# Kernel optimization log

Measured on AMD Instinct MI355X. Metric: run time of the kernel, lower is better.

Reference implementation:

```python
import jax, jax.numpy as jnp
import numpy as np

N_NODES = 100000
LN_EPS = 1e-5


def gcn_conv(x, src, dst, W, b, num_nodes):
    """PyG-style GCNConv: x@W, add self-loops, symmetric D^-1/2 A D^-1/2 aggregation, + bias."""
    h = x @ W  # [N, out]
    loop = jnp.arange(num_nodes, dtype=src.dtype)
    s = jnp.concatenate([src, loop])
    d = jnp.concatenate([dst, loop])
    deg = jax.ops.segment_sum(jnp.ones_like(d, dtype=h.dtype), d, num_segments=num_nodes)
    dinv = jnp.where(deg > 0, jax.lax.rsqrt(deg), 0.0)
    norm = dinv[s] * dinv[d]  # [E+N]
    msg = h[s] * norm[:, None]
    return jax.ops.segment_sum(msg, d, num_segments=num_nodes) + b


def layer_norm(x, g, b):
    mu = jnp.mean(x, axis=-1, keepdims=True)
    var = jnp.mean(jnp.square(x - mu), axis=-1, keepdims=True)
    return (x - mu) * jax.lax.rsqrt(var + LN_EPS) * g + b


def setup_inputs() -> dict:
    key = jax.random.key(0)
    ks = jax.random.split(key, 12)
    N, D, OUT = N_NODES, 128, 16
    E, EL = 1600000, 500000
    x = jnp.arange(N, dtype=jnp.int64) if jax.config.jax_enable_x64 else jnp.arange(N, dtype=jnp.int32)
    edge_index = jax.random.randint(ks[0], (2, E), 0, N)
    edge_label_index = jax.random.randint(ks[1], (2, EL), 0, N)
    s = 1.0 / np.sqrt(D)
    return {
        "x": x,
        "edge_index": edge_index,
        "edge_label_index": edge_label_index,
        "emb_table": jax.random.normal(ks[2], (N, D), jnp.float32),
        "W1": jax.random.normal(ks[3], (D, D), jnp.float32) * s,
        "b1": jnp.zeros((D,), jnp.float32),
        "ln_g": jnp.ones((D,), jnp.float32),
        "ln_b": jnp.zeros((D,), jnp.float32),
        "W2": jax.random.normal(ks[4], (D, OUT), jnp.float32) * s,
        "b2": jnp.zeros((OUT,), jnp.float32),
        "L1": jax.random.normal(ks[5], (2 * OUT, 16), jnp.float32) * (1.0 / np.sqrt(2 * OUT)),
        "bl1": jnp.zeros((16,), jnp.float32),
        "L2": jax.random.normal(ks[6], (16, 1), jnp.float32) * 0.25,
        "bl2": jnp.zeros((1,), jnp.float32),
    }


def reference(x, edge_index, edge_label_index, emb_table, W1, b1, ln_g, ln_b, W2, b2, L1, bl1, L2, bl2):
    src, dst = edge_index[0], edge_index[1]
    h = emb_table[x]  # embed + squeeze -> [N, D]
    # conv 1: GCN -> relu -> (dropout, eval: identity) -> LayerNorm
    h = gcn_conv(h, src, dst, W1, b1, N_NODES)
    h = layer_norm(jax.nn.relu(h), ln_g, ln_b)
    # conv 2: emb is the pre-activation output (what encode returns)
    z = gcn_conv(h, src, dst, W2, b2, N_NODES)  # [N, 16]
    # decode: gather-concat + small MLP (dropout eval: identity)
    feat = jnp.concatenate([z[edge_label_index[0]], z[edge_label_index[1]]], axis=-1)  # [EL, 32]
    out = jax.nn.relu(feat @ L1 + bl1) if False else (feat @ L1 + bl1)  # Sequential has no activation
    out = out @ L2 + bl2  # [EL, 1]
    return out
```

## Files before the change

### kernel.cpp

```cpp
#include <hip/hip_runtime.h>


typedef __attribute__((ext_vector_type(8))) __bf16 bf16x8;
typedef __attribute__((ext_vector_type(4))) __bf16 bf16x4;
typedef __attribute__((ext_vector_type(4))) float f32x4;

static __device__ __forceinline__ unsigned f2bf1(float x) {
  unsigned u = __float_as_uint(x);
  return (u + 0x7FFFu + ((u >> 16) & 1u)) >> 16;
}
static __device__ __forceinline__ unsigned packbf2(float lo, float hi) {
  return f2bf1(lo) | (f2bf1(hi) << 16);
}
static __device__ __forceinline__ float bfl(unsigned u) { return __uint_as_float(u << 16); }
static __device__ __forceinline__ float bfh(unsigned u) { return __uint_as_float(u & 0xFFFF0000u); }

__global__ __launch_bounds__(256) void prep_wfrag(const float* __restrict__ W1,
                                                  ushort* __restrict__ wfrag) {
  int idx = blockIdx.x * 256 + threadIdx.x;
  int j = idx & 7, lane = (idx >> 3) & 63, ct = (idx >> 9) & 7, kt = idx >> 12;
  int k = kt * 32 + (lane >> 4) * 8 + j;
  int col = ct * 16 + (lane & 15);
  __bf16 h = (__bf16)W1[k * 128 + col];
  wfrag[idx] = __builtin_bit_cast(ushort, h);
}

__global__ __launch_bounds__(256) void bucket_edges(const int* __restrict__ src,
                                                    const int* __restrict__ dst,
                                                    int E, int NB,
                                                    int* __restrict__ qcur,
                                                    uint2* __restrict__ queues,
                                                    int qcap) {
  __shared__ int lcnt[128];
  __shared__ int lbase[128];
  int t = threadIdx.x;
  int CH = (E + gridDim.x - 1) / gridDim.x;
  int beg = blockIdx.x * CH;
  int end = min(E, beg + CH);
  for (int i = t; i < NB; i += 256) lcnt[i] = 0;
  __syncthreads();
  for (int e = beg + t; e < end; e += 256) atomicAdd(&lcnt[dst[e] >> 10], 1);
  __syncthreads();
  for (int i = t; i < NB; i += 256) {
    lbase[i] = atomicAdd(&qcur[i], lcnt[i]);
    lcnt[i] = 0;
  }
  __syncthreads();
  for (int e = beg + t; e < end; e += 256) {
    int d = dst[e];
    int p = d >> 10;
    int pos = lbase[p] + atomicAdd(&lcnt[p], 1);
    if (pos < qcap) queues[(size_t)p * qcap + pos] = make_uint2((unsigned)src[e], (unsigned)d);
  }
}

__global__ __launch_bounds__(1024) void scatter_ell(const uint2* __restrict__ queues,
                                                    const int* __restrict__ qcur,
                                                    int qcap, int* __restrict__ cnt,
                                                    float* __restrict__ dinv,
                                                    int* __restrict__ colsrc, int N) {
  __shared__ int lcnt[1024];
  int b = blockIdx.x, t = threadIdx.x;
  lcnt[t] = 0;
  __syncthreads();
  int len = min(qcur[b], qcap);
  const uint2* q = queues + (size_t)b * qcap;
  int lo = b << 10;
  for (int i = t; i < len; i += 1024) {
    uint2 e = q[i];
    int pos = atomicAdd(&lcnt[e.y - lo], 1);
    if (pos < 64) colsrc[(size_t)e.y * 64 + pos] = (int)e.x;
  }
  __syncthreads();
  int node = lo + t;
  if (node < N) {
    int c = min(lcnt[t], 64);
    cnt[node] = c;
    dinv[node] = rsqrtf((float)(c + 1));
  }
}

__global__ __launch_bounds__(256) void gemm1_mfma(
    const int* __restrict__ x, const float* __restrict__ emb,
    const ushort* __restrict__ wfrag, const float* __restrict__ dinv,
    unsigned* __restrict__ h1b, int N) {
  __shared__ alignas(16) ushort Wlds[16384];
  int t = threadIdx.x;
  for (int i = t; i < 2048; i += 256)
    ((uint4*)Wlds)[i] = ((const uint4*)wfrag)[i];
  __syncthreads();
  int w = t >> 6, lane = t & 63;
  int row0 = blockIdx.x * 128 + w * 32;
  int rB = lane & 15, kg = lane >> 4;
  int n0 = row0 + rB, n1 = row0 + 16 + rB;
  const float* e0 = emb + (size_t)x[min(n0, N - 1)] * 128 + kg * 8;
  const float* e1 = emb + (size_t)x[min(n1, N - 1)] * 128 + kg * 8;
  f32x4 acc[2][8];
#pragma unroll
  for (int g = 0; g < 2; ++g)
#pragma unroll
    for (int ct = 0; ct < 8; ++ct) acc[g][ct] = (f32x4)(0.f);
#pragma unroll
  for (int kt = 0; kt < 4; ++kt) {
    float4 p0 = *(const float4*)(e0 + kt * 32);
    float4 p1 = *(const float4*)(e0 + kt * 32 + 4);
    float4 q0 = *(const float4*)(e1 + kt * 32);
    float4 q1 = *(const float4*)(e1 + kt * 32 + 4);
    bf16x8 fb0, fb1;
    fb0[0] = (__bf16)p0.x; fb0[1] = (__bf16)p0.y; fb0[2] = (__bf16)p0.z; fb0[3] = (__bf16)p0.w;
    fb0[4] = (__bf16)p1.x; fb0[5] = (__bf16)p1.y; fb0[6] = (__bf16)p1.z; fb0[7] = (__bf16)p1.w;
    fb1[0] = (__bf16)q0.x; fb1[1] = (__bf16)q0.y; fb1[2] = (__bf16)q0.z; fb1[3] = (__bf16)q0.w;
    fb1[4] = (__bf16)q1.x; fb1[5] = (__bf16)q1.y; fb1[6] = (__bf16)q1.z; fb1[7] = (__bf16)q1.w;
#pragma unroll
    for (int ct = 0; ct < 8; ++ct) {
      bf16x8 wv = *(const bf16x8*)&Wlds[((kt * 8 + ct) * 64 + lane) * 8];
      acc[0][ct] = __builtin_amdgcn_mfma_f32_16x16x32_bf16(wv, fb0, acc[0][ct], 0, 0, 0);
      acc[1][ct] = __builtin_amdgcn_mfma_f32_16x16x32_bf16(wv, fb1, acc[1][ct], 0, 0, 0);
    }
  }
#pragma unroll
  for (int g = 0; g < 2; ++g) {
    int node = row0 + g * 16 + rB;
    if (node < N) {
      float dv = dinv[node];
#pragma unroll
      for (int ct = 0; ct < 8; ++ct) {
        f32x4 a = acc[g][ct];
        bf16x4 o;
        o[0] = (__bf16)(a[0] * dv); o[1] = (__bf16)(a[1] * dv);
        o[2] = (__bf16)(a[2] * dv); o[3] = (__bf16)(a[3] * dv);
        *(uint2*)&h1b[(size_t)node * 64 + ct * 8 + kg * 2] = __builtin_bit_cast(uint2, o);
      }
    }
  }
}

__global__ __launch_bounds__(256) void agg1_ln(const unsigned* __restrict__ h1b,
                                               const int* __restrict__ cnt_a,
                                               const int* __restrict__ colsrc,
                                               const float* __restrict__ dinv,
                                               const float* __restrict__ b1,
                                               const float* __restrict__ lng,
                                               const float* __restrict__ lnb,
                                               unsigned* __restrict__ h2b, int N) {
  int v = blockIdx.x * 4 + (threadIdx.x >> 6);
  int lane = threadIdx.x & 63;
  if (v >= N) return;
  int g = lane >> 4, dq = lane & 15;
  const uint4* tb = (const uint4*)h1b;
  int myidx = colsrc[(size_t)v * 64 + lane];
  int cnt = cnt_a[v];
  float a0 = 0.f, a1 = 0.f, a2 = 0.f, a3 = 0.f;
  float a4 = 0.f, a5 = 0.f, a6 = 0.f, a7 = 0.f;
#define ACC1(m)                                              \
  {                                                          \
    a0 += bfl(m.x); a1 += bfh(m.x); a2 += bfl(m.y);          \
    a3 += bfh(m.y); a4 += bfl(m.z); a5 += bfh(m.z);          \
    a6 += bfl(m.w); a7 += bfh(m.w);                          \
  }
  if (g == 0) {
    uint4 ms = tb[(size_t)v * 16 + dq];
    ACC1(ms);
  }
  int i = 0;
  for (; i + 8 <= cnt; i += 8) {
    int s0 = __shfl(myidx, i + g, 64);
    int s1 = __shfl(myidx, i + 4 + g, 64);
    uint4 m0 = tb[(size_t)s0 * 16 + dq];
    uint4 m1 = tb[(size_t)s1 * 16 + dq];
    ACC1(m0);
    ACC1(m1);
  }
  for (; i < cnt; i += 4) {
    int slot = i + g;
    int s = __shfl(myidx, min(slot, cnt - 1), 64);
    uint4 m = tb[(size_t)s * 16 + dq];
    if (slot < cnt) ACC1(m);
  }
#undef ACC1
#pragma unroll
  for (int off = 16; off < 64; off <<= 1) {
    a0 += __shfl_xor(a0, off, 64);
    a1 += __shfl_xor(a1, off, 64);
    a2 += __shfl_xor(a2, off, 64);
    a3 += __shfl_xor(a3, off, 64);
    a4 += __shfl_xor(a4, off, 64);
    a5 += __shfl_xor(a5, off, 64);
    a6 += __shfl_xor(a6, off, 64);
    a7 += __shfl_xor(a7, off, 64);
  }
  float dv = dinv[v];
  float4 bb0 = ((const float4*)b1)[dq * 2];
  float4 bb1 = ((const float4*)b1)[dq * 2 + 1];
  float v0 = fmaxf(a0 * dv + bb0.x, 0.f);
  float v1 = fmaxf(a1 * dv + bb0.y, 0.f);
  float v2 = fmaxf(a2 * dv + bb0.z, 0.f);
  float v3 = fmaxf(a3 * dv + bb0.w, 0.f);
  float v4 = fmaxf(a4 * dv + bb1.x, 0.f);
  float v5 = fmaxf(a5 * dv + bb1.y, 0.f);
  float v6 = fmaxf(a6 * dv + bb1.z, 0.f);
  float v7 = fmaxf(a7 * dv + bb1.w, 0.f);
  float s1 = ((v0 + v1) + (v2 + v3)) + ((v4 + v5) + (v6 + v7));
  float s2 = ((v0 * v0 + v1 * v1) + (v2 * v2 + v3 * v3)) +
             ((v4 * v4 + v5 * v5) + (v6 * v6 + v7 * v7));
#pragma unroll
  for (int off = 1; off < 16; off <<= 1) {
    s1 += __shfl_xor(s1, off, 64);
    s2 += __shfl_xor(s2, off, 64);
  }
  float mu = s1 * (1.f / 128.f);
  float var = s2 * (1.f / 128.f) - mu * mu;
  float rs = rsqrtf(var + 1e-5f);
  if (g == 0) {
    float4 gg0 = ((const float4*)lng)[dq * 2];
    float4 gg1 = ((const float4*)lng)[dq * 2 + 1];
    float4 nb0 = ((const float4*)lnb)[dq * 2];
    float4 nb1 = ((const float4*)lnb)[dq * 2 + 1];
    uint4 o;
    o.x = packbf2((v0 - mu) * rs * gg0.x + nb0.x, (v1 - mu) * rs * gg0.y + nb0.y);
    o.y = packbf2((v2 - mu) * rs * gg0.z + nb0.z, (v3 - mu) * rs * gg0.w + nb0.w);
    o.z = packbf2((v4 - mu) * rs * gg1.x + nb1.x, (v5 - mu) * rs * gg1.y + nb1.y);
    o.w = packbf2((v6 - mu) * rs * gg1.z + nb1.z, (v7 - mu) * rs * gg1.w + nb1.w);
    ((uint4*)h2b)[(size_t)v * 16 + dq] = o;
  }
}

__global__ __launch_bounds__(256) void gemm2(const unsigned* __restrict__ h2b,
                                             const float* __restrict__ W2,
                                             const float* __restrict__ dinv,
                                             unsigned* __restrict__ zsb, int N) {
  __shared__ float W2s[128 * 16];
  int t = threadIdx.x;
#pragma unroll
  for (int i = 0; i < 8; ++i) W2s[t + i * 256] = W2[t + i * 256];
  __syncthreads();
  int cp = t & 7, r = t >> 3;
  for (int rb = blockIdx.x * 32; rb < N; rb += gridDim.x * 32) {
    int row = rb + r;
    if (row >= N) continue;
    const uint4* xr = (const uint4*)(h2b + (size_t)row * 64);
    float a0 = 0.f, a1 = 0.f;
#pragma unroll
    for (int k8 = 0; k8 < 16; ++k8) {
      uint4 u = xr[k8];
      float f0 = bfl(u.x), f1 = bfh(u.x), f2 = bfl(u.y), f3 = bfh(u.y);
      float f4 = bfl(u.z), f5 = bfh(u.z), f6 = bfl(u.w), f7 = bfh(u.w);
      int kb = k8 * 8;
      float2 w;
      w = ((const float2*)W2s)[(kb + 0) * 8 + cp]; a0 += f0 * w.x; a1 += f0 * w.y;
      w = ((const float2*)W2s)[(kb + 1) * 8 + cp]; a0 += f1 * w.x; a1 += f1 * w.y;
      w = ((const float2*)W2s)[(kb + 2) * 8 + cp]; a0 += f2 * w.x; a1 += f2 * w.y;
      w = ((const float2*)W2s)[(kb + 3) * 8 + cp]; a0 += f3 * w.x; a1 += f3 * w.y;
      w = ((const float2*)W2s)[(kb + 4) * 8 + cp]; a0 += f4 * w.x; a1 += f4 * w.y;
      w = ((const float2*)W2s)[(kb + 5) * 8 + cp]; a0 += f5 * w.x; a1 += f5 * w.y;
      w = ((const float2*)W2s)[(kb + 6) * 8 + cp]; a0 += f6 * w.x; a1 += f6 * w.y;
      w = ((const float2*)W2s)[(kb + 7) * 8 + cp]; a0 += f7 * w.x; a1 += f7 * w.y;
    }
    float dv = dinv[row];
    zsb[(size_t)row * 8 + cp] = packbf2(a0 * dv, a1 * dv);
  }
}

__global__ __launch_bounds__(256) void agg2(const unsigned* __restrict__ zsb,
                                            const int* __restrict__ cnt_a,
                                            const int* __restrict__ colsrc,
                                            const float* __restrict__ dinv,
                                            const float* __restrict__ b2,
                                            unsigned* __restrict__ zb, int N) {
  int v = blockIdx.x * 4 + (threadIdx.x >> 6);
  int lane = threadIdx.x & 63;
  if (v >= N) return;
  int g = lane >> 2, q = lane & 3;
  const uint2* tb = (const uint2*)zsb;
  int myidx = colsrc[(size_t)v * 64 + lane];
  int cnt = cnt_a[v];
  float a0 = 0.f, a1 = 0.f, a2 = 0.f, a3 = 0.f;
  if (g == 0) {
    uint2 m = tb[(size_t)v * 4 + q];
    a0 = bfl(m.x); a1 = bfh(m.x); a2 = bfl(m.y); a3 = bfh(m.y);
  }
  for (int i = 0; i < cnt; i += 16) {
    int slot = i + g;
    int s = __shfl(myidx, min(slot, cnt - 1), 64);
    uint2 m = tb[(size_t)s * 4 + q];
    if (slot < cnt) {
      a0 += bfl(m.x); a1 += bfh(m.x); a2 += bfl(m.y); a3 += bfh(m.y);
    }
  }
#pragma unroll
  for (int off = 4; off < 64; off <<= 1) {
    a0 += __shfl_xor(a0, off, 64);
    a1 += __shfl_xor(a1, off, 64);
    a2 += __shfl_xor(a2, off, 64);
    a3 += __shfl_xor(a3, off, 64);
  }
  if (g == 0) {
    float dv = dinv[v];
    float4 bb = ((const float4*)b2)[q];
    uint2 o;
    o.x = packbf2(a0 * dv + bb.x, a1 * dv + bb.y);
    o.y = packbf2(a2 * dv + bb.z, a3 * dv + bb.w);
    ((uint2*)zb)[(size_t)v * 4 + q] = o;
  }
}

__global__ __launch_bounds__(256) void decode(const int* __restrict__ eli,
                                              const unsigned* __restrict__ zb,
                                              const float* __restrict__ L1,
                                              const float* __restrict__ bl1,
                                              const float* __restrict__ L2,
                                              const float* __restrict__ bl2,
                                              float* __restrict__ out, int EL) {
  __shared__ float L1s[32 * 16];
  __shared__ float L2s[16];
  __shared__ float bl1s[16];
  __shared__ float bl2s;
  int t = threadIdx.x;
  L1s[t] = L1[t];
  L1s[256 + t] = L1[256 + t];
  if (t < 16) { L2s[t] = L2[t]; bl1s[t] = bl1[t]; }
  if (t == 0) bl2s = bl2[0];
  __syncthreads();
  int l = blockIdx.x * 256 + t;
  if (l >= EL) return;
  int a = eli[l], b = eli[EL + l];
  const uint4* zt = (const uint4*)zb;
  uint4 ua0 = zt[(size_t)a * 2], ua1 = zt[(size_t)a * 2 + 1];
  uint4 ub0 = zt[(size_t)b * 2], ub1 = zt[(size_t)b * 2 + 1];
  float fa[16], fb[16];
  fa[0] = bfl(ua0.x); fa[1] = bfh(ua0.x); fa[2] = bfl(ua0.y); fa[3] = bfh(ua0.y);
  fa[4] = bfl(ua0.z); fa[5] = bfh(ua0.z); fa[6] = bfl(ua0.w); fa[7] = bfh(ua0.w);
  fa[8] = bfl(ua1.x); fa[9] = bfh(ua1.x); fa[10] = bfl(ua1.y); fa[11] = bfh(ua1.y);
  fa[12] = bfl(ua1.z); fa[13] = bfh(ua1.z); fa[14] = bfl(ua1.w); fa[15] = bfh(ua1.w);
  fb[0] = bfl(ub0.x); fb[1] = bfh(ub0.x); fb[2] = bfl(ub0.y); fb[3] = bfh(ub0.y);
  fb[4] = bfl(ub0.z); fb[5] = bfh(ub0.z); fb[6] = bfl(ub0.w); fb[7] = bfh(ub0.w);
  fb[8] = bfl(ub1.x); fb[9] = bfh(ub1.x); fb[10] = bfl(ub1.y); fb[11] = bfh(ub1.y);
  fb[12] = bfl(ub1.z); fb[13] = bfh(ub1.z); fb[14] = bfl(ub1.w); fb[15] = bfh(ub1.w);
  float h[16];
#pragma unroll
  for (int j = 0; j < 16; ++j) h[j] = bl1s[j];
#pragma unroll
  for (int k = 0; k < 16; ++k) {
#pragma unroll
    for (int j = 0; j < 16; ++j) {
      h[j] += fa[k] * L1s[k * 16 + j];
      h[j] += fb[k] * L1s[(16 + k) * 16 + j];
    }
  }
  float o = bl2s;
#pragma unroll
  for (int j = 0; j < 16; ++j) o += h[j] * L2s[j];
  out[l] = o;
}

extern "C" void kernel_launch(void* const* d_in, const int* in_sizes, int n_in,
                              void* d_out, int out_size, void* d_ws, size_t ws_size,
                              hipStream_t stream) {
  const int* x = (const int*)d_in[0];
  const int* ei = (const int*)d_in[1];
  const int* eli = (const int*)d_in[2];
  const float* emb = (const float*)d_in[3];
  const float* W1 = (const float*)d_in[4];
  const float* b1 = (const float*)d_in[5];
  const float* lng = (const float*)d_in[6];
  const float* lnb = (const float*)d_in[7];
  const float* W2 = (const float*)d_in[8];
  const float* b2 = (const float*)d_in[9];
  const float* L1 = (const float*)d_in[10];
  const float* bl1 = (const float*)d_in[11];
  const float* L2 = (const float*)d_in[12];
  const float* bl2 = (const float*)d_in[13];

  int N = in_sizes[0];
  int E = in_sizes[1] / 2;
  int EL = in_sizes[2] / 2;
  const int* src = ei;
  const int* dst = ei + E;

  int NB = (N + 1023) >> 10;
  int qcap = E / NB + 4096;

  char* ws = (char*)d_ws;
  auto align256 = [](size_t v) { return (v + 255) & ~(size_t)255; };
  size_t p = 0;
  int* qcur = (int*)(ws + p); p += 4096;
  int* cnt = (int*)(ws + p); p += align256((size_t)N * 4);
  float* dinv = (float*)(ws + p); p += align256((size_t)N * 4);
  ushort* wfrag = (ushort*)(ws + p); p += align256(16384 * 2);
  int* colsrc = (int*)(ws + p); p += align256((size_t)N * 64 * 4);
  uint2* queues = (uint2*)(ws + p); p += align256((size_t)NB * qcap * 8);
  unsigned* h1b = (unsigned*)(ws + p); p += align256((size_t)N * 64 * 4);
  unsigned* h2b = (unsigned*)(ws + p); p += align256((size_t)N * 64 * 4);
  unsigned* zsb = (unsigned*)(ws + p); p += align256((size_t)N * 8 * 4);
  unsigned* zb = (unsigned*)(ws + p); p += align256((size_t)N * 8 * 4);
  (void)ws_size; (void)n_in; (void)out_size;

  hipMemsetAsync(qcur, 0, 4096, stream);

  prep_wfrag<<<64, 256, 0, stream>>>(W1, wfrag);
  bucket_edges<<<512, 256, 0, stream>>>(src, dst, E, NB, qcur, queues, qcap);
  scatter_ell<<<NB, 1024, 0, stream>>>(queues, qcur, qcap, cnt, dinv, colsrc, N);
  gemm1_mfma<<<(N + 127) / 128, 256, 0, stream>>>(x, emb, wfrag, dinv, h1b, N);
  agg1_ln<<<(N + 3) / 4, 256, 0, stream>>>(h1b, cnt, colsrc, dinv, b1, lng, lnb, h2b, N);
  gemm2<<<512, 256, 0, stream>>>(h2b, W2, dinv, zsb, N);
  agg2<<<(N + 3) / 4, 256, 0, stream>>>(zsb, cnt, colsrc, dinv, b2, zb, N);
  decode<<<(EL + 255) / 256, 256, 0, stream>>>(eli, zb, L1, bl1, L2, bl2,
                                               (float*)d_out, EL);
}
```

Baseline: 202.9 us.

## Split layer-1 aggregation by feature half and fold LayerNorm into gemm2

The layer-1 aggregation kernel is split into two blocks per node group, each gathering half of the 128 features, so more blocks run and each gathers eight neighbours per step. LayerNorm is no longer applied there: the kernel writes pre-normalisation ReLU outputs plus partial sum and sum-of-squares per half. gemm2 rebuilds mean and variance and applies the normalisation algebraically through gamma-scaled W2 and precomputed gamma·W2 and beta·W2 column sums from a new prep kernel. The aim is to spread the gather across more blocks and move the LN arithmetic into the small GEMM, at the cost of reading each neighbour's index list twice and rounding un-normalised values to bf16.

```diff
diff --git a/kernel.cpp b/kernel.cpp
--- a/kernel.cpp
+++ b/kernel.cpp
@@ -23,6 +23,26 @@
   int col = ct * 16 + (lane & 15);
   __bf16 h = (__bf16)W1[k * 128 + col];
   wfrag[idx] = __builtin_bit_cast(ushort, h);
+}
+
+__global__ __launch_bounds__(256) void prep_w2(const float* __restrict__ W2,
+                                               const float* __restrict__ lng,
+                                               const float* __restrict__ lnb,
+                                               float* __restrict__ W2g,
+                                               float* __restrict__ gW2c,
+                                               float* __restrict__ bW2c) {
+  int t = threadIdx.x;
+  for (int i = t; i < 2048; i += 256) W2g[i] = lng[i >> 4] * W2[i];
+  if (t < 16) {
+    float ga = 0.f, ba = 0.f;
+    for (int k = 0; k < 128; ++k) {
+      float w = W2[k * 16 + t];
+      ga += lng[k] * w;
+      ba += lnb[k] * w;
+    }
+    gW2c[t] = ga;
+    bW2c[t] = ba;
+  }
 }
 
 __global__ __launch_bounds__(256) void bucket_edges(const int* __restrict__ src,
@@ -135,18 +155,20 @@
   }
 }
 
-__global__ __launch_bounds__(256) void agg1_ln(const unsigned* __restrict__ h1b,
-                                               const int* __restrict__ cnt_a,
-                                               const int* __restrict__ colsrc,
-                                               const float* __restrict__ dinv,
-                                               const float* __restrict__ b1,
-                                               const float* __restrict__ lng,
-                                               const float* __restrict__ lnb,
-                                               unsigned* __restrict__ h2b, int N) {
-  int v = blockIdx.x * 4 + (threadIdx.x >> 6);
+__global__ __launch_bounds__(256) void agg1_half(const unsigned* __restrict__ h1b,
+                                                 const int* __restrict__ cnt_a,
+                                                 const int* __restrict__ colsrc,
+                                                 const float* __restrict__ dinv,
+                                                 const float* __restrict__ b1,
+                                                 unsigned* __restrict__ pre,
+                                                 float2* __restrict__ s12, int N) {
+  int bid = blockIdx.x;
+  int ng = bid >> 1, h = bid & 1;
+  int v = ng * 4 + (threadIdx.x >> 6);
   int lane = threadIdx.x & 63;
   if (v >= N) return;
-  int g = lane >> 4, dq = lane & 15;
+  int g = lane >> 3, dq = lane & 7;
+  int hoff = h * 8;
   const uint4* tb = (const uint4*)h1b;
   int myidx = colsrc[(size_t)v * 64 + lane];
   int cnt = cnt_a[v];
@@ -159,27 +181,27 @@
     a6 += bfl(m.w); a7 += bfh(m.w);                          \
   }
   if (g == 0) {
-    uint4 ms = tb[(size_t)v * 16 + dq];
+    uint4 ms = tb[(size_t)v * 16 + hoff + dq];
     ACC1(ms);
   }
   int i = 0;
-  for (; i + 8 <= cnt; i += 8) {
+  for (; i + 16 <= cnt; i += 16) {
     int s0 = __shfl(myidx, i + g, 64);
-    int s1 = __shfl(myidx, i + 4 + g, 64);
-    uint4 m0 = tb[(size_t)s0 * 16 + dq];
-    uint4 m1 = tb[(size_t)s1 * 16 + dq];
+    int s1_ = __shfl(myidx, i + 8 + g, 64);
+    uint4 m0 = tb[(size_t)s0 * 16 + hoff + dq];
+    uint4 m1 = tb[(size_t)s1_ * 16 + hoff + dq];
     ACC1(m0);
     ACC1(m1);
   }
-  for (; i < cnt; i += 4) {
+  for (; i < cnt; i += 8) {
     int slot = i + g;
     int s = __shfl(myidx, min(slot, cnt - 1), 64);
-    uint4 m = tb[(size_t)s * 16 + dq];
+    uint4 m = tb[(size_t)s * 16 + hoff + dq];
     if (slot < cnt) ACC1(m);
   }
 #undef ACC1
 #pragma unroll
-  for (int off = 16; off < 64; off <<= 1) {
+  for (int off = 8; off < 64; off <<= 1) {
     a0 += __shfl_xor(a0, off, 64);
     a1 += __shfl_xor(a1, off, 64);
     a2 += __shfl_xor(a2, off, 64);
@@ -190,8 +212,8 @@
     a7 += __shfl_xor(a7, off, 64);
   }
   float dv = dinv[v];
-  float4 bb0 = ((const float4*)b1)[dq * 2];
-  float4 bb1 = ((const float4*)b1)[dq * 2 + 1];
+  float4 bb0 = ((const float4*)b1)[h * 16 + dq * 2];
+  float4 bb1 = ((const float4*)b1)[h * 16 + dq * 2 + 1];
   float v0 = fmaxf(a0 * dv + bb0.x, 0.f);
   float v1 = fmaxf(a1 * dv + bb0.y, 0.f);
   float v2 = fmaxf(a2 * dv + bb0.z, 0.f);
@@ -204,41 +226,45 @@
   float s2 = ((v0 * v0 + v1 * v1) + (v2 * v2 + v3 * v3)) +
              ((v4 * v4 + v5 * v5) + (v6 * v6 + v7 * v7));
 #pragma unroll
-  for (int off = 1; off < 16; off <<= 1) {
+  for (int off = 1; off < 8; off <<= 1) {
     s1 += __shfl_xor(s1, off, 64);
     s2 += __shfl_xor(s2, off, 64);
   }
-  float mu = s1 * (1.f / 128.f);
-  float var = s2 * (1.f / 128.f) - mu * mu;
-  float rs = rsqrtf(var + 1e-5f);
   if (g == 0) {
-    float4 gg0 = ((const float4*)lng)[dq * 2];
-    float4 gg1 = ((const float4*)lng)[dq * 2 + 1];
-    float4 nb0 = ((const float4*)lnb)[dq * 2];
-    float4 nb1 = ((const float4*)lnb)[dq * 2 + 1];
     uint4 o;
-    o.x = packbf2((v0 - mu) * rs * gg0.x + nb0.x, (v1 - mu) * rs * gg0.y + nb0.y);
-    o.y = packbf2((v2 - mu) * rs * gg0.z + nb0.z, (v3 - mu) * rs * gg0.w + nb0.w);
-    o.z = packbf2((v4 - mu) * rs * gg1.x + nb1.x, (v5 - mu) * rs * gg1.y + nb1.y);
-    o.w = packbf2((v6 - mu) * rs * gg1.z + nb1.z, (v7 - mu) * rs * gg1.w + nb1.w);
-    ((uint4*)h2b)[(size_t)v * 16 + dq] = o;
-  }
-}
-
-__global__ __launch_bounds__(256) void gemm2(const unsigned* __restrict__ h2b,
-                                             const float* __restrict__ W2,
+    o.x = packbf2(v0, v1);
+    o.y = packbf2(v2, v3);
+    o.z = packbf2(v4, v5);
+    o.w = packbf2(v6, v7);
+    ((uint4*)pre)[(size_t)v * 16 + hoff + dq] = o;
+    if (dq == 0) s12[((size_t)v << 1) | h] = make_float2(s1, s2);
+  }
+}
+
+__global__ __launch_bounds__(256) void gemm2(const unsigned* __restrict__ pre,
+                                             const float2* __restrict__ s12,
+                                             const float* __restrict__ W2g,
+                                             const float* __restrict__ gW2c,
+                                             const float* __restrict__ bW2c,
                                              const float* __restrict__ dinv,
                                              unsigned* __restrict__ zsb, int N) {
   __shared__ float W2s[128 * 16];
+  __shared__ float gws[16], bws[16];
   int t = threadIdx.x;
 #pragma unroll
-  for (int i = 0; i < 8; ++i) W2s[t + i * 256] = W2[t + i * 256];
+  for (int i = 0; i < 8; ++i) W2s[t + i * 256] = W2g[t + i * 256];
+  if (t < 16) { gws[t] = gW2c[t]; bws[t] = bW2c[t]; }
   __syncthreads();
   int cp = t & 7, r = t >> 3;
   for (int rb = blockIdx.x * 32; rb < N; rb += gridDim.x * 32) {
     int row = rb + r;
     if (row >= N) continue;
-    const uint4* xr = (const uint4*)(h2b + (size_t)row * 64);
+    const uint4* xr = (const uint4*)(pre + (size_t)row * 64);
+    float2 A = s12[(size_t)row * 2], B = s12[(size_t)row * 2 + 1];
+    float sa = A.x + B.x, sb = A.y + B.y;
+    float mu = sa * (1.f / 128.f);
+    float var = sb * (1.f / 128.f) - mu * mu;
+    float rs = rsqrtf(var + 1e-5f);
     float a0 = 0.f, a1 = 0.f;
 #pragma unroll
     for (int k8 = 0; k8 < 16; ++k8) {
@@ -256,8 +282,12 @@
       w = ((const float2*)W2s)[(kb + 6) * 8 + cp]; a0 += f6 * w.x; a1 += f6 * w.y;
       w = ((const float2*)W2s)[(kb + 7) * 8 + cp]; a0 += f7 * w.x; a1 += f7 * w.y;
     }
+    float2 gw = ((const float2*)gws)[cp];
+    float2 bw = ((const float2*)bws)[cp];
     float dv = dinv[row];
-    zsb[(size_t)row * 8 + cp] = packbf2(a0 * dv, a1 * dv);
+    float z0 = (rs * (a0 - mu * gw.x) + bw.x) * dv;
+    float z1 = (rs * (a1 - mu * gw.y) + bw.y) * dv;
+    zsb[(size_t)row * 8 + cp] = packbf2(z0, z1);
   }
 }
 
@@ -387,10 +417,14 @@
   int* cnt = (int*)(ws + p); p += align256((size_t)N * 4);
   float* dinv = (float*)(ws + p); p += align256((size_t)N * 4);
   ushort* wfrag = (ushort*)(ws + p); p += align256(16384 * 2);
+  float* W2g = (float*)(ws + p); p += align256(2048 * 4);
+  float* gW2c = (float*)(ws + p); p += 256;
+  float* bW2c = (float*)(ws + p); p += 256;
   int* colsrc = (int*)(ws + p); p += align256((size_t)N * 64 * 4);
   uint2* queues = (uint2*)(ws + p); p += align256((size_t)NB * qcap * 8);
   unsigned* h1b = (unsigned*)(ws + p); p += align256((size_t)N * 64 * 4);
-  unsigned* h2b = (unsigned*)(ws + p); p += align256((size_t)N * 64 * 4);
+  unsigned* pre = (unsigned*)(ws + p); p += align256((size_t)N * 64 * 4);
+  float2* s12 = (float2*)(ws + p); p += align256((size_t)N * 2 * 8);
   unsigned* zsb = (unsigned*)(ws + p); p += align256((size_t)N * 8 * 4);
   unsigned* zb = (unsigned*)(ws + p); p += align256((size_t)N * 8 * 4);
   (void)ws_size; (void)n_in; (void)out_size;
@@ -398,11 +432,12 @@
   hipMemsetAsync(qcur, 0, 4096, stream);
 
   prep_wfrag<<<64, 256, 0, stream>>>(W1, wfrag);
+  prep_w2<<<1, 256, 0, stream>>>(W2, lng, lnb, W2g, gW2c, bW2c);
   bucket_edges<<<512, 256, 0, stream>>>(src, dst, E, NB, qcur, queues, qcap);
   scatter_ell<<<NB, 1024, 0, stream>>>(queues, qcur, qcap, cnt, dinv, colsrc, N);
   gemm1_mfma<<<(N + 127) / 128, 256, 0, stream>>>(x, emb, wfrag, dinv, h1b, N);
-  agg1_ln<<<(N + 3) / 4, 256, 0, stream>>>(h1b, cnt, colsrc, dinv, b1, lng, lnb, h2b, N);
-  gemm2<<<512, 256, 0, stream>>>(h2b, W2, dinv, zsb, N);
+  agg1_half<<<((N + 3) / 4) * 2, 256, 0, stream>>>(h1b, cnt, colsrc, dinv, b1, pre, s12, N);
+  gemm2<<<512, 256, 0, stream>>>(pre, s12, W2g, gW2c, bW2c, dinv, zsb, N);
   agg2<<<(N + 3) / 4, 256, 0, stream>>>(zsb, cnt, colsrc, dinv, b2, zb, N);
   decode<<<(EL + 255) / 256, 256, 0, stream>>>(eli, zb, L1, bl1, L2, bl2,
                                                (float*)d_out, EL);
```

New measurement: 226.6 us. 11.7% more time.

## Fuse LayerNorm and second GEMM into aggregation kernel via folded LN weights

Applied to the files above, without the earlier changes.

Folds the LayerNorm affine parameters into W2 (W2g = g*W2, plus column sums g·W2 and b·W2) in a prep kernel, so the second linear layer can be computed directly from pre-normalized values inside agg1_ln using the mean and rstd. This removes the h2b intermediate buffer (N x 128 bf16 write and read) and the separate gemm2 launch. It also skips loading colsrc entries beyond each node's count. The fused epilogue adds per-wave float4 weight loads and shuffle reductions, and the algebraic folding slightly changes rounding because the bf16 quantisation of h2 is no longer applied.

```diff
diff --git a/kernel.cpp b/kernel.cpp
--- a/kernel.cpp
+++ b/kernel.cpp
@@ -15,14 +15,35 @@
 static __device__ __forceinline__ float bfl(unsigned u) { return __uint_as_float(u << 16); }
 static __device__ __forceinline__ float bfh(unsigned u) { return __uint_as_float(u & 0xFFFF0000u); }
 
-__global__ __launch_bounds__(256) void prep_wfrag(const float* __restrict__ W1,
-                                                  ushort* __restrict__ wfrag) {
-  int idx = blockIdx.x * 256 + threadIdx.x;
-  int j = idx & 7, lane = (idx >> 3) & 63, ct = (idx >> 9) & 7, kt = idx >> 12;
-  int k = kt * 32 + (lane >> 4) * 8 + j;
-  int col = ct * 16 + (lane & 15);
-  __bf16 h = (__bf16)W1[k * 128 + col];
-  wfrag[idx] = __builtin_bit_cast(ushort, h);
+__global__ __launch_bounds__(256) void prep(const float* __restrict__ W1,
+                                            const float* __restrict__ W2,
+                                            const float* __restrict__ lng,
+                                            const float* __restrict__ lnb,
+                                            ushort* __restrict__ wfrag,
+                                            float* __restrict__ W2g,
+                                            float* __restrict__ gW2c,
+                                            float* __restrict__ bW2c) {
+  int t = threadIdx.x;
+  if (blockIdx.x < 64) {
+    int idx = blockIdx.x * 256 + t;
+    int j = idx & 7, lane = (idx >> 3) & 63, ct = (idx >> 9) & 7, kt = idx >> 12;
+    int k = kt * 32 + (lane >> 4) * 8 + j;
+    int col = ct * 16 + (lane & 15);
+    __bf16 h = (__bf16)W1[k * 128 + col];
+    wfrag[idx] = __builtin_bit_cast(ushort, h);
+  } else {
+    for (int i = t; i < 2048; i += 256) W2g[i] = lng[i >> 4] * W2[i];
+    if (t < 16) {
+      float ga = 0.f, ba = 0.f;
+      for (int k = 0; k < 128; ++k) {
+        float w = W2[k * 16 + t];
+        ga += lng[k] * w;
+        ba += lnb[k] * w;
+      }
+      gW2c[t] = ga;
+      bW2c[t] = ba;
+    }
+  }
 }
 
 __global__ __launch_bounds__(256) void bucket_edges(const int* __restrict__ src,
@@ -140,16 +161,17 @@
                                                const int* __restrict__ colsrc,
                                                const float* __restrict__ dinv,
                                                const float* __restrict__ b1,
-                                               const float* __restrict__ lng,
-                                               const float* __restrict__ lnb,
-                                               unsigned* __restrict__ h2b, int N) {
+                                               const float* __restrict__ W2g,
+                                               const float* __restrict__ gW2c,
+                                               const float* __restrict__ bW2c,
+                                               unsigned* __restrict__ zsb, int N) {
   int v = blockIdx.x * 4 + (threadIdx.x >> 6);
   int lane = threadIdx.x & 63;
   if (v >= N) return;
   int g = lane >> 4, dq = lane & 15;
   const uint4* tb = (const uint4*)h1b;
-  int myidx = colsrc[(size_t)v * 64 + lane];
   int cnt = cnt_a[v];
+  int myidx = (lane < cnt) ? colsrc[(size_t)v * 64 + lane] : 0;
   float a0 = 0.f, a1 = 0.f, a2 = 0.f, a3 = 0.f;
   float a4 = 0.f, a5 = 0.f, a6 = 0.f, a7 = 0.f;
 #define ACC1(m)                                              \
@@ -165,9 +187,9 @@
   int i = 0;
   for (; i + 8 <= cnt; i += 8) {
     int s0 = __shfl(myidx, i + g, 64);
-    int s1 = __shfl(myidx, i + 4 + g, 64);
+    int s1_ = __shfl(myidx, i + 4 + g, 64);
     uint4 m0 = tb[(size_t)s0 * 16 + dq];
-    uint4 m1 = tb[(size_t)s1 * 16 + dq];
+    uint4 m1 = tb[(size_t)s1_ * 16 + dq];
     ACC1(m0);
     ACC1(m1);
   }
@@ -211,53 +233,35 @@
   float mu = s1 * (1.f / 128.f);
   float var = s2 * (1.f / 128.f) - mu * mu;
   float rs = rsqrtf(var + 1e-5f);
-  if (g == 0) {
-    float4 gg0 = ((const float4*)lng)[dq * 2];
-    float4 gg1 = ((const float4*)lng)[dq * 2 + 1];
-    float4 nb0 = ((const float4*)lnb)[dq * 2];
-    float4 nb1 = ((const float4*)lnb)[dq * 2 + 1];
-    uint4 o;
-    o.x = packbf2((v0 - mu) * rs * gg0.x + nb0.x, (v1 - mu) * rs * gg0.y + nb0.y);
-    o.y = packbf2((v2 - mu) * rs * gg0.z + nb0.z, (v3 - mu) * rs * gg0.w + nb0.w);
-    o.z = packbf2((v4 - mu) * rs * gg1.x + nb1.x, (v5 - mu) * rs * gg1.y + nb1.y);
-    o.w = packbf2((v6 - mu) * rs * gg1.z + nb1.z, (v7 - mu) * rs * gg1.w + nb1.w);
-    ((uint4*)h2b)[(size_t)v * 16 + dq] = o;
-  }
-}
-
-__global__ __launch_bounds__(256) void gemm2(const unsigned* __restrict__ h2b,
-                                             const float* __restrict__ W2,
-                                             const float* __restrict__ dinv,
-                                             unsigned* __restrict__ zsb, int N) {
-  __shared__ float W2s[128 * 16];
-  int t = threadIdx.x;
-#pragma unroll
-  for (int i = 0; i < 8; ++i) W2s[t + i * 256] = W2[t + i * 256];
-  __syncthreads();
-  int cp = t & 7, r = t >> 3;
-  for (int rb = blockIdx.x * 32; rb < N; rb += gridDim.x * 32) {
-    int row = rb + r;
-    if (row >= N) continue;
-    const uint4* xr = (const uint4*)(h2b + (size_t)row * 64);
-    float a0 = 0.f, a1 = 0.f;
-#pragma unroll
-    for (int k8 = 0; k8 < 16; ++k8) {
-      uint4 u = xr[k8];
-      float f0 = bfl(u.x), f1 = bfh(u.x), f2 = bfl(u.y), f3 = bfh(u.y);
-      float f4 = bfl(u.z), f5 = bfh(u.z), f6 = bfl(u.w), f7 = bfh(u.w);
-      int kb = k8 * 8;
-      float2 w;
-      w = ((const float2*)W2s)[(kb + 0) * 8 + cp]; a0 += f0 * w.x; a1 += f0 * w.y;
-      w = ((const float2*)W2s)[(kb + 1) * 8 + cp]; a0 += f1 * w.x; a1 += f1 * w.y;
-      w = ((const float2*)W2s)[(kb + 2) * 8 + cp]; a0 += f2 * w.x; a1 += f2 * w.y;
-      w = ((const float2*)W2s)[(kb + 3) * 8 + cp]; a0 += f3 * w.x; a1 += f3 * w.y;
-      w = ((const float2*)W2s)[(kb + 4) * 8 + cp]; a0 += f4 * w.x; a1 += f4 * w.y;
-      w = ((const float2*)W2s)[(kb + 5) * 8 + cp]; a0 += f5 * w.x; a1 += f5 * w.y;
-      w = ((const float2*)W2s)[(kb + 6) * 8 + cp]; a0 += f6 * w.x; a1 += f6 * w.y;
-      w = ((const float2*)W2s)[(kb + 7) * 8 + cp]; a0 += f7 * w.x; a1 += f7 * w.y;
-    }
-    float dv = dinv[row];
-    zsb[(size_t)row * 8 + cp] = packbf2(a0 * dv, a1 * dv);
+  float p0 = 0.f, p1 = 0.f, p2 = 0.f, p3 = 0.f;
+  const float* wbase = W2g + (size_t)(dq * 8) * 16 + g * 4;
+  float vv[8] = {v0, v1, v2, v3, v4, v5, v6, v7};
+#pragma unroll
+  for (int j = 0; j < 8; ++j) {
+    float4 w = *(const float4*)(wbase + j * 16);
+    p0 += vv[j] * w.x;
+    p1 += vv[j] * w.y;
+    p2 += vv[j] * w.z;
+    p3 += vv[j] * w.w;
+  }
+#pragma unroll
+  for (int off = 1; off < 16; off <<= 1) {
+    p0 += __shfl_xor(p0, off, 64);
+    p1 += __shfl_xor(p1, off, 64);
+    p2 += __shfl_xor(p2, off, 64);
+    p3 += __shfl_xor(p3, off, 64);
+  }
+  if (dq == 0) {
+    float4 gw = ((const float4*)gW2c)[g];
+    float4 bw = ((const float4*)bW2c)[g];
+    float z0 = (rs * (p0 - mu * gw.x) + bw.x) * dv;
+    float z1 = (rs * (p1 - mu * gw.y) + bw.y) * dv;
+    float z2 = (rs * (p2 - mu * gw.z) + bw.z) * dv;
+    float z3 = (rs * (p3 - mu * gw.w) + bw.w) * dv;
+    uint2 o;
+    o.x = packbf2(z0, z1);
+    o.y = packbf2(z2, z3);
+    ((uint2*)zsb)[(size_t)v * 4 + g] = o;
   }
 }
 
@@ -272,8 +276,8 @@
   if (v >= N) return;
   int g = lane >> 2, q = lane & 3;
   const uint2* tb = (const uint2*)zsb;
-  int myidx = colsrc[(size_t)v * 64 + lane];
   int cnt = cnt_a[v];
+  int myidx = (lane < cnt) ? colsrc[(size_t)v * 64 + lane] : 0;
   float a0 = 0.f, a1 = 0.f, a2 = 0.f, a3 = 0.f;
   if (g == 0) {
     uint2 m = tb[(size_t)v * 4 + q];
@@ -387,22 +391,24 @@
   int* cnt = (int*)(ws + p); p += align256((size_t)N * 4);
   float* dinv = (float*)(ws + p); p += align256((size_t)N * 4);
   ushort* wfrag = (ushort*)(ws + p); p += align256(16384 * 2);
+  float* W2g = (float*)(ws + p); p += align256(2048 * 4);
+  float* gW2c = (float*)(ws + p); p += 256;
+  float* bW2c = (float*)(ws + p); p += 256;
   int* colsrc = (int*)(ws + p); p += align256((size_t)N * 64 * 4);
   uint2* queues = (uint2*)(ws + p); p += align256((size_t)NB * qcap * 8);
   unsigned* h1b = (unsigned*)(ws + p); p += align256((size_t)N * 64 * 4);
-  unsigned* h2b = (unsigned*)(ws + p); p += align256((size_t)N * 64 * 4);
   unsigned* zsb = (unsigned*)(ws + p); p += align256((size_t)N * 8 * 4);
   unsigned* zb = (unsigned*)(ws + p); p += align256((size_t)N * 8 * 4);
   (void)ws_size; (void)n_in; (void)out_size;
 
   hipMemsetAsync(qcur, 0, 4096, stream);
 
-  prep_wfrag<<<64, 256, 0, stream>>>(W1, wfrag);
+  prep<<<65, 256, 0, stream>>>(W1, W2, lng, lnb, wfrag, W2g, gW2c, bW2c);
   bucket_edges<<<512, 256, 0, stream>>>(src, dst, E, NB, qcur, queues, qcap);
   scatter_ell<<<NB, 1024, 0, stream>>>(queues, qcur, qcap, cnt, dinv, colsrc, N);
   gemm1_mfma<<<(N + 127) / 128, 256, 0, stream>>>(x, emb, wfrag, dinv, h1b, N);
-  agg1_ln<<<(N + 3) / 4, 256, 0, stream>>>(h1b, cnt, colsrc, dinv, b1, lng, lnb, h2b, N);
-  gemm2<<<512, 256, 0, stream>>>(h2b, W2, dinv, zsb, N);
+  agg1_ln<<<(N + 3) / 4, 256, 0, stream>>>(h1b, cnt, colsrc, dinv, b1, W2g, gW2c,
+                                           bW2c, zsb, N);
   agg2<<<(N + 3) / 4, 256, 0, stream>>>(zsb, cnt, colsrc, dinv, b2, zb, N);
   decode<<<(EL + 255) / 256, 256, 0, stream>>>(eli, zb, L1, bl1, L2, bl2,
                                                (float*)d_out, EL);
```

Measured after the change: 251.9 us. +24.1%, slower.
